# Performance work log

Measured on AMD Instinct MI355X. Metric: run time of the kernel, lower is better.

Reference implementation:

```python
import jax, jax.numpy as jnp
import numpy as np

LEVEL = 256
BLOCKS = 8
THRESH = 10.0


def setup_inputs() -> dict:
    key = jax.random.key(0)
    img = jax.random.randint(key, (16, 1024, 1024), 0, LEVEL).astype(jnp.float32)
    return {"img": img}


def _clahe(img):
    B, H, W = img.shape
    bm, bn = H // BLOCKS, W // BLOCKS
    v = img.astype(jnp.int32)  # pixel values 0..255, used as histogram bins

    # ---- per-block histograms via one flat scatter-add (segment_sum) ----
    bi = jnp.arange(H) // bm                      # block row per pixel row
    bj = jnp.arange(W) // bn                      # block col per pixel col
    blk = bi[:, None] * BLOCKS + bj[None, :]      # [H, W] block id
    seg = (jnp.arange(B)[:, None, None] * (BLOCKS * BLOCKS) + blk[None]) * LEVEL + v
    hists = jax.ops.segment_sum(
        jnp.ones((B * H * W,), jnp.float32), seg.reshape(-1),
        num_segments=B * BLOCKS * BLOCKS * LEVEL)
    hists = hists.reshape(B, BLOCKS, BLOCKS, LEVEL)

    # ---- clip histogram: redistribute excess above threshold uniformly ----
    # threshold_value = sum(hists)/LEVEL*threshold ; block sum is bm*bn exactly
    tv = (bm * bn) / LEVEL * THRESH
    total_extra = jnp.sum(jnp.maximum(hists - tv, 0.0), axis=-1, keepdims=True)
    mean_extra = total_extra / LEVEL
    # int() truncation of non-negative values == floor
    clip = jnp.floor(jnp.where(hists >= tv, tv + mean_extra, hists + mean_extra))

    # ---- CDF -> uint8 mapping table per block ----
    cdf = jnp.cumsum(clip, axis=-1) * ((LEVEL - 1) / (bm * bn))
    maps = (jnp.floor(cdf).astype(jnp.int32) % 256).astype(jnp.float32)  # [B,BLOCKS,BLOCKS,LEVEL]

    # ---- per-pixel bilinear blend of 2x2 neighboring block maps ----
    ii = jnp.arange(H, dtype=jnp.float32)
    jj = jnp.arange(W, dtype=jnp.float32)
    # Python int() truncates toward zero, so r,c are always >= 0
    r = jnp.trunc((ii - bm / 2) / bm).astype(jnp.int32)   # [H]
    c = jnp.trunc((jj - bn / 2) / bn).astype(jnp.int32)   # [W]
    x1 = (ii - (r.astype(jnp.float32) + 0.5) * bm) / bm   # [H]
    y1 = (jj - (c.astype(jnp.float32) + 0.5) * bn) / bn   # [W]
    rp = jnp.minimum(r + 1, BLOCKS - 1)
    cp = jnp.minimum(c + 1, BLOCKS - 1)
    # on last block row/col the original falls back to 1-D / nearest interp:
    x1e = jnp.where(r >= BLOCKS - 1, 0.0, x1)[:, None]    # [H,1]
    y1e = jnp.where(c >= BLOCKS - 1, 0.0, y1)[None, :]    # [1,W]

    bidx = jnp.arange(B)[:, None, None]

    def gather(rr, cc):  # maps[b, rr[i], cc[j], v[b,i,j]] -> [B,H,W]
        return maps[bidx, rr[None, :, None], cc[None, None, :], v]

    lu = gather(r, c)
    lb = gather(rp, c)
    ru = gather(r, cp)
    rb = gather(rp, cp)
    out = (1 - y1e) * ((1 - x1e) * lu + x1e * lb) + y1e * ((1 - x1e) * ru + x1e * rb)
    # final .astype('uint8') cast
    return (jnp.trunc(out).astype(jnp.int32) % 256).astype(jnp.float32)


def reference(img) -> jnp.ndarray:
    return _clahe(img)
```

## Files before the change

kernel.cpp:

```cpp
#include <hip/hip_runtime.h>
#include <hip/hip_bf16.h>

#define LEVEL 256
#define BLOCKS 8

__global__ __launch_bounds__(256) void clahe_hist_kernel(const float* __restrict__ img,
                                                         float* __restrict__ maps,
                                                         unsigned char* __restrict__ u8img) {
    __shared__ int   hist[256];
    __shared__ float red[256];
    __shared__ float scan[256];
    __shared__ float s_me;

    const int t   = threadIdx.x;
    const int bid = blockIdx.x;
    const int b   = bid >> 6;
    const int blk = bid & 63;
    const int br  = blk >> 3;
    const int bc  = blk & 7;

    hist[t] = 0;
    __syncthreads();

    const size_t base = (size_t)b * 1048576 + (size_t)(br * 128) * 1024 + (size_t)(bc * 128);
    const float* p = img + base;
    unsigned char* q8 = u8img ? (u8img + base) : nullptr;
    for (int it = 0; it < 16; ++it) {
        int idx = it * 256 + t;
        int y   = idx >> 5;
        int x   = (idx & 31) * 4;
        float4 v = *(const float4*)(p + (size_t)y * 1024 + x);
        int va = (int)v.x, vb = (int)v.y, vc = (int)v.z, vd = (int)v.w;
        atomicAdd(&hist[va], 1);
        atomicAdd(&hist[vb], 1);
        atomicAdd(&hist[vc], 1);
        atomicAdd(&hist[vd], 1);
        if (q8) {
            uchar4 pk;
            pk.x = (unsigned char)va; pk.y = (unsigned char)vb;
            pk.z = (unsigned char)vc; pk.w = (unsigned char)vd;
            *(uchar4*)(q8 + (size_t)y * 1024 + x) = pk;
        }
    }
    __syncthreads();

    const float tv = 640.0f;
    float h = (float)hist[t];
    float extra = fmaxf(h - tv, 0.0f);
    red[t] = extra;
    __syncthreads();
    for (int off = 128; off > 0; off >>= 1) {
        if (t < off) red[t] += red[t + off];
        __syncthreads();
    }
    if (t == 0) s_me = red[0] * (1.0f / 256.0f);
    __syncthreads();
    const float me = s_me;
    float clip = floorf(((h >= tv) ? tv : h) + me);

    scan[t] = clip;
    __syncthreads();
    for (int off = 1; off < 256; off <<= 1) {
        float add = (t >= off) ? scan[t - off] : 0.0f;
        __syncthreads();
        scan[t] += add;
        __syncthreads();
    }
    float cdf = scan[t] * (255.0f / 16384.0f);
    int m = ((int)floorf(cdf)) & 255;
    maps[(size_t)bid * 256 + t] = (float)m;
}

template <bool U8>
__global__ __launch_bounds__(256) void clahe_map_kernel(const float* __restrict__ imgf,
                                                        const unsigned char* __restrict__ img8,
                                                        const float* __restrict__ maps,
                                                        float* __restrict__ out) {
#pragma clang fp contract(off)
    __shared__ float4 m4[256];

    const int t  = threadIdx.x;
    const int b  = blockIdx.z;
    const int i0 = blockIdx.y * 64;
    const int j0 = blockIdx.x * 64;

    const int r  = (i0 >= 64) ? ((i0 - 64) >> 7) : 0;
    const int c  = (j0 >= 64) ? ((j0 - 64) >> 7) : 0;
    const int rp = min(r + 1, BLOCKS - 1);
    const int cp = min(c + 1, BLOCKS - 1);
    const bool rEdge = (r >= BLOCKS - 1);
    const bool cEdge = (c >= BLOCKS - 1);

    const float* mb = maps + (size_t)b * 64 * 256;
    {
        float lu = mb[(r  * 8 + c ) * 256 + t];
        float lb = mb[(rp * 8 + c ) * 256 + t];
        float ru = mb[(r  * 8 + cp) * 256 + t];
        float rb = mb[(rp * 8 + cp) * 256 + t];
        m4[t] = make_float4(lu, lb, ru, rb);
    }
    __syncthreads();

    const size_t ibase = (size_t)b * 1048576;
    const int row_in = t >> 4;
    const int col4   = (t & 15) * 4;

    for (int it = 0; it < 4; ++it) {
        const int i = i0 + it * 16 + row_in;
        const int j = j0 + col4;

        int vv[4];
        if (U8) {
            uchar4 px = *(const uchar4*)(img8 + ibase + (size_t)i * 1024 + j);
            vv[0] = px.x; vv[1] = px.y; vv[2] = px.z; vv[3] = px.w;
        } else {
            float4 px = *(const float4*)(imgf + ibase + (size_t)i * 1024 + j);
            vv[0] = (int)px.x; vv[1] = (int)px.y; vv[2] = (int)px.z; vv[3] = (int)px.w;
        }

        const float x1  = rEdge ? 0.0f : ((float)i - (float)(r * 128 + 64)) * 0.0078125f;
        const float x0  = 1.0f - x1;

        float4 o4;
        float* ov = (float*)&o4;
        for (int k = 0; k < 4; ++k) {
            const int jj = j + k;
            const float y1 = cEdge ? 0.0f : ((float)jj - (float)(c * 128 + 64)) * 0.0078125f;
            const float4 q = m4[vv[k]];
            float o = (1.0f - y1) * (x0 * q.x + x1 * q.y)
                    + y1 * (x0 * q.z + x1 * q.w);
            ov[k] = (float)(((int)o) & 255);
        }
        *(float4*)(out + ibase + (size_t)i * 1024 + j) = o4;
    }
}

extern "C" void kernel_launch(void* const* d_in, const int* in_sizes, int n_in,
                              void* d_out, int out_size, void* d_ws, size_t ws_size,
                              hipStream_t stream) {
    const float* img = (const float*)d_in[0];
    float* out = (float*)d_out;
    float* maps = (float*)d_ws;

    const size_t maps_bytes = (size_t)1024 * 256 * sizeof(float);
    const size_t u8_bytes   = (size_t)16 * 1024 * 1024;
    const bool use_u8 = ws_size >= maps_bytes + u8_bytes;
    unsigned char* u8img = use_u8 ? ((unsigned char*)d_ws + maps_bytes) : nullptr;

    clahe_hist_kernel<<<dim3(1024), dim3(256), 0, stream>>>(img, maps, u8img);
    if (use_u8) {
        clahe_map_kernel<true><<<dim3(16, 16, 16), dim3(256), 0, stream>>>(
            nullptr, u8img, maps, out);
    } else {
        clahe_map_kernel<false><<<dim3(16, 16, 16), dim3(256), 0, stream>>>(
            img, nullptr, maps, out);
    }
}
```

Before: 124.1 us.

## Pack block maps as bytes and widen map-kernel tiles to 64x128

```diff
diff --git a/kernel.cpp b/kernel.cpp
--- a/kernel.cpp
+++ b/kernel.cpp
@@ -1,11 +1,10 @@
 #include <hip/hip_runtime.h>
-#include <hip/hip_bf16.h>
 
 #define LEVEL 256
 #define BLOCKS 8
 
 __global__ __launch_bounds__(256) void clahe_hist_kernel(const float* __restrict__ img,
-                                                         float* __restrict__ maps,
+                                                         unsigned char* __restrict__ maps8,
                                                          unsigned char* __restrict__ u8img) {
     __shared__ int   hist[256];
     __shared__ float red[256];
@@ -68,70 +67,110 @@
     }
     float cdf = scan[t] * (255.0f / 16384.0f);
     int m = ((int)floorf(cdf)) & 255;
-    maps[(size_t)bid * 256 + t] = (float)m;
+    maps8[(size_t)bid * 256 + t] = (unsigned char)m;
 }
 
 template <bool U8>
 __global__ __launch_bounds__(256) void clahe_map_kernel(const float* __restrict__ imgf,
                                                         const unsigned char* __restrict__ img8,
-                                                        const float* __restrict__ maps,
+                                                        const unsigned char* __restrict__ maps8,
                                                         float* __restrict__ out) {
 #pragma clang fp contract(off)
-    __shared__ float4 m4[256];
+    __shared__ unsigned int mL[256];
+    __shared__ unsigned int mR[256];
 
     const int t  = threadIdx.x;
     const int b  = blockIdx.z;
     const int i0 = blockIdx.y * 64;
-    const int j0 = blockIdx.x * 64;
+    const int j0 = blockIdx.x * 128;
 
     const int r  = (i0 >= 64) ? ((i0 - 64) >> 7) : 0;
-    const int c  = (j0 >= 64) ? ((j0 - 64) >> 7) : 0;
     const int rp = min(r + 1, BLOCKS - 1);
-    const int cp = min(c + 1, BLOCKS - 1);
     const bool rEdge = (r >= BLOCKS - 1);
-    const bool cEdge = (c >= BLOCKS - 1);
 
-    const float* mb = maps + (size_t)b * 64 * 256;
+    const int cL  = (j0 >= 64) ? ((j0 - 64) >> 7) : 0;
+    const int cR  = j0 >> 7;
+    const int cLp = min(cL + 1, BLOCKS - 1);
+    const int cRp = min(cR + 1, BLOCKS - 1);
+    const bool cLEdge = (cL >= BLOCKS - 1);
+    const bool cREdge = (cR >= BLOCKS - 1);
+
+    const unsigned char* mb = maps8 + (size_t)b * 64 * 256;
     {
-        float lu = mb[(r  * 8 + c ) * 256 + t];
-        float lb = mb[(rp * 8 + c ) * 256 + t];
-        float ru = mb[(r  * 8 + cp) * 256 + t];
-        float rb = mb[(rp * 8 + cp) * 256 + t];
-        m4[t] = make_float4(lu, lb, ru, rb);
+        unsigned lu = mb[(r  * 8 + cL ) * 256 + t];
+        unsigned lb = mb[(rp * 8 + cL ) * 256 + t];
+        unsigned ru = mb[(r  * 8 + cLp) * 256 + t];
+        unsigned rb = mb[(rp * 8 + cLp) * 256 + t];
+        mL[t] = lu | (lb << 8) | (ru << 16) | (rb << 24);
+        unsigned lu2 = mb[(r  * 8 + cR ) * 256 + t];
+        unsigned lb2 = mb[(rp * 8 + cR ) * 256 + t];
+        unsigned ru2 = mb[(r  * 8 + cRp) * 256 + t];
+        unsigned rb2 = mb[(rp * 8 + cRp) * 256 + t];
+        mR[t] = lu2 | (lb2 << 8) | (ru2 << 16) | (rb2 << 24);
     }
     __syncthreads();
 
     const size_t ibase = (size_t)b * 1048576;
-    const int row_in = t >> 4;
-    const int col4   = (t & 15) * 4;
+    const float rbase = (float)(r * 128 + 64);
+    const float cbaseL = (float)(cL * 128 + 64);
+    const float cbaseR = (float)(cR * 128 + 64);
 
-    for (int it = 0; it < 4; ++it) {
-        const int i = i0 + it * 16 + row_in;
-        const int j = j0 + col4;
+#pragma unroll
+    for (int it = 0; it < 2; ++it) {
+        const int idx = it * 256 + t;
+        const int row = idx >> 3;
+        const int cu  = (idx & 7) * 16;
+        const int i   = i0 + row;
+        const int j   = j0 + cu;
+        const int half = cu >> 6;
+        const unsigned int* mt = half ? mR : mL;
+        const bool  cE    = half ? cREdge : cLEdge;
+        const float cbase = half ? cbaseR : cbaseL;
 
-        int vv[4];
+        unsigned int w[4];
         if (U8) {
-            uchar4 px = *(const uchar4*)(img8 + ibase + (size_t)i * 1024 + j);
-            vv[0] = px.x; vv[1] = px.y; vv[2] = px.z; vv[3] = px.w;
+            uint4 px = *(const uint4*)(img8 + ibase + (size_t)i * 1024 + j);
+            w[0] = px.x; w[1] = px.y; w[2] = px.z; w[3] = px.w;
         } else {
-            float4 px = *(const float4*)(imgf + ibase + (size_t)i * 1024 + j);
-            vv[0] = (int)px.x; vv[1] = (int)px.y; vv[2] = (int)px.z; vv[3] = (int)px.w;
+            const float* pf = imgf + ibase + (size_t)i * 1024 + j;
+#pragma unroll
+            for (int q = 0; q < 4; ++q) {
+                float4 f = *(const float4*)(pf + q * 4);
+                w[q] = (((unsigned)(int)f.x) & 255u)
+                     | ((((unsigned)(int)f.y) & 255u) << 8)
+                     | ((((unsigned)(int)f.z) & 255u) << 16)
+                     | ((((unsigned)(int)f.w) & 255u) << 24);
+            }
         }
 
-        const float x1  = rEdge ? 0.0f : ((float)i - (float)(r * 128 + 64)) * 0.0078125f;
-        const float x0  = 1.0f - x1;
+        const float x1 = rEdge ? 0.0f : ((float)i - rbase) * 0.0078125f;
+        const float x0 = 1.0f - x1;
 
-        float4 o4;
-        float* ov = (float*)&o4;
-        for (int k = 0; k < 4; ++k) {
-            const int jj = j + k;
-            const float y1 = cEdge ? 0.0f : ((float)jj - (float)(c * 128 + 64)) * 0.0078125f;
-            const float4 q = m4[vv[k]];
-            float o = (1.0f - y1) * (x0 * q.x + x1 * q.y)
-                    + y1 * (x0 * q.z + x1 * q.w);
-            ov[k] = (float)(((int)o) & 255);
+        float o16[16];
+#pragma unroll
+        for (int q = 0; q < 4; ++q) {
+            const unsigned int wq = w[q];
+#pragma unroll
+            for (int k = 0; k < 4; ++k) {
+                const int v = (wq >> (8 * k)) & 255;
+                const unsigned m = mt[v];
+                const float lu = (float)(m & 255u);
+                const float lb = (float)((m >> 8) & 255u);
+                const float ru = (float)((m >> 16) & 255u);
+                const float rb = (float)(m >> 24);
+                const float jj = (float)(j + q * 4 + k);
+                const float y1 = cE ? 0.0f : (jj - cbase) * 0.0078125f;
+                float o = (1.0f - y1) * (x0 * lu + x1 * lb)
+                        + y1 * (x0 * ru + x1 * rb);
+                o16[q * 4 + k] = (float)(((int)o) & 255);
+            }
         }
-        *(float4*)(out + ibase + (size_t)i * 1024 + j) = o4;
+
+        float* po = out + ibase + (size_t)i * 1024 + j;
+        *(float4*)(po +  0) = make_float4(o16[ 0], o16[ 1], o16[ 2], o16[ 3]);
+        *(float4*)(po +  4) = make_float4(o16[ 4], o16[ 5], o16[ 6], o16[ 7]);
+        *(float4*)(po +  8) = make_float4(o16[ 8], o16[ 9], o16[10], o16[11]);
+        *(float4*)(po + 12) = make_float4(o16[12], o16[13], o16[14], o16[15]);
     }
 }
 
@@ -140,19 +179,19 @@
                               hipStream_t stream) {
     const float* img = (const float*)d_in[0];
     float* out = (float*)d_out;
-    float* maps = (float*)d_ws;
 
-    const size_t maps_bytes = (size_t)1024 * 256 * sizeof(float);
+    unsigned char* maps8 = (unsigned char*)d_ws;
+    const size_t maps_bytes = (size_t)1024 * 256;
     const size_t u8_bytes   = (size_t)16 * 1024 * 1024;
     const bool use_u8 = ws_size >= maps_bytes + u8_bytes;
     unsigned char* u8img = use_u8 ? ((unsigned char*)d_ws + maps_bytes) : nullptr;
 
-    clahe_hist_kernel<<<dim3(1024), dim3(256), 0, stream>>>(img, maps, u8img);
+    clahe_hist_kernel<<<dim3(1024), dim3(256), 0, stream>>>(img, maps8, u8img);
     if (use_u8) {
-        clahe_map_kernel<true><<<dim3(16, 16, 16), dim3(256), 0, stream>>>(
-            nullptr, u8img, maps, out);
+        clahe_map_kernel<true><<<dim3(8, 16, 16), dim3(256), 0, stream>>>(
+            nullptr, u8img, maps8, out);
     } else {
-        clahe_map_kernel<false><<<dim3(16, 16, 16), dim3(256), 0, stream>>>(
-            img, nullptr, maps, out);
+        clahe_map_kernel<false><<<dim3(8, 16, 16), dim3(256), 0, stream>>>(
+            img, nullptr, maps8, out);
     }
 }
```

After: 130.4 us. 5.1% more time.

## Fuse histogram and mapping into one cooperative kernel with grid sync

Applied to the files above, without the earlier changes.

```diff
diff --git a/kernel.cpp b/kernel.cpp
--- a/kernel.cpp
+++ b/kernel.cpp
@@ -1,11 +1,141 @@
 #include <hip/hip_runtime.h>
-#include <hip/hip_bf16.h>
+#include <hip/hip_cooperative_groups.h>
+
+namespace cg = cooperative_groups;
 
 #define LEVEL 256
 #define BLOCKS 8
 
+__global__ __launch_bounds__(256, 4) void clahe_fused(const float* __restrict__ img,
+                                                      float* __restrict__ out,
+                                                      unsigned char* __restrict__ maps8) {
+#pragma clang fp contract(off)
+    __shared__ unsigned int pix[4096];
+    __shared__ int   hist[256];
+    __shared__ float red[256];
+    __shared__ float scan[256];
+    __shared__ unsigned int tab[1024];
+    __shared__ float s_me;
+
+    const int t   = threadIdx.x;
+    const int bid = blockIdx.x;
+    const int b   = bid >> 6;
+    const int br  = (bid >> 3) & 7;
+    const int bc  = bid & 7;
+
+    hist[t] = 0;
+    __syncthreads();
+
+    const size_t base = (size_t)b * 1048576 + (size_t)(br * 128) * 1024 + (size_t)(bc * 128);
+    const float* p = img + base;
+#pragma unroll 4
+    for (int it = 0; it < 16; ++it) {
+        int idx = it * 256 + t;
+        int y   = idx >> 5;
+        int x   = (idx & 31) * 4;
+        float4 v = *(const float4*)(p + (size_t)y * 1024 + x);
+        int va = (int)v.x, vb = (int)v.y, vc = (int)v.z, vd = (int)v.w;
+        atomicAdd(&hist[va], 1);
+        atomicAdd(&hist[vb], 1);
+        atomicAdd(&hist[vc], 1);
+        atomicAdd(&hist[vd], 1);
+        pix[idx] = (unsigned)va | ((unsigned)vb << 8) | ((unsigned)vc << 16) | ((unsigned)vd << 24);
+    }
+    __syncthreads();
+
+    const float tv = 640.0f;
+    float h = (float)hist[t];
+    red[t] = fmaxf(h - tv, 0.0f);
+    __syncthreads();
+    for (int off = 128; off > 0; off >>= 1) {
+        if (t < off) red[t] += red[t + off];
+        __syncthreads();
+    }
+    if (t == 0) s_me = red[0] * (1.0f / 256.0f);
+    __syncthreads();
+    const float me = s_me;
+    float clip = floorf(((h >= tv) ? tv : h) + me);
+
+    scan[t] = clip;
+    __syncthreads();
+    for (int off = 1; off < 256; off <<= 1) {
+        float add = (t >= off) ? scan[t - off] : 0.0f;
+        __syncthreads();
+        scan[t] += add;
+        __syncthreads();
+    }
+    float cdf = scan[t] * (255.0f / 16384.0f);
+    int m = ((int)floorf(cdf)) & 255;
+    maps8[(size_t)bid * 256 + t] = (unsigned char)m;
+
+    __threadfence();
+    cg::this_grid().sync();
+    __threadfence();
+
+    const int r0 = (br > 0) ? (br - 1) : 0;
+    const int r1 = br;
+    const int c0 = (bc > 0) ? (bc - 1) : 0;
+    const int c1 = bc;
+    const unsigned char* mb = maps8 + (size_t)b * 16384;
+#pragma unroll
+    for (int q = 0; q < 4; ++q) {
+        int rq  = (q & 2) ? r1 : r0;
+        int cq  = (q & 1) ? c1 : c0;
+        int rpq = min(rq + 1, BLOCKS - 1);
+        int cpq = min(cq + 1, BLOCKS - 1);
+        unsigned lu = mb[(rq  * 8 + cq ) * 256 + t];
+        unsigned lb = mb[(rpq * 8 + cq ) * 256 + t];
+        unsigned ru = mb[(rq  * 8 + cpq) * 256 + t];
+        unsigned rb = mb[(rpq * 8 + cpq) * 256 + t];
+        tab[q * 256 + t] = lu | (lb << 8) | (ru << 16) | (rb << 24);
+    }
+    __syncthreads();
+
+    const int colq = (t & 31) * 4;
+    const int qj   = colq >> 6;
+    const int cq   = qj ? c1 : c0;
+    const bool cEdge = (cq >= BLOCKS - 1);
+    const float cbase = (float)(cq * 128 + 64);
+    const int jg = bc * 128 + colq;
+    float y1v[4], y0v[4];
+#pragma unroll
+    for (int k = 0; k < 4; ++k) {
+        y1v[k] = cEdge ? 0.0f : ((float)(jg + k) - cbase) * 0.0078125f;
+        y0v[k] = 1.0f - y1v[k];
+    }
+
+#pragma unroll
+    for (int it = 0; it < 16; ++it) {
+        const int qi  = (it >= 8) ? 1 : 0;
+        const int rq  = qi ? r1 : r0;
+        const bool rEdge = (rq >= BLOCKS - 1);
+        const int row = it * 8 + (t >> 5);
+        const int ig  = br * 128 + row;
+        const float x1 = rEdge ? 0.0f : ((float)ig - (float)(rq * 128 + 64)) * 0.0078125f;
+        const float x0 = 1.0f - x1;
+
+        const unsigned w = pix[it * 256 + t];
+        const unsigned* tb = &tab[(qi * 2 + qj) * 256];
+
+        float4 o4;
+        float* ov = (float*)&o4;
+#pragma unroll
+        for (int k = 0; k < 4; ++k) {
+            const int v = (w >> (8 * k)) & 255;
+            const unsigned mm = tb[v];
+            const float lu = (float)(mm & 255u);
+            const float lb = (float)((mm >> 8) & 255u);
+            const float ru = (float)((mm >> 16) & 255u);
+            const float rb = (float)(mm >> 24);
+            float o = y0v[k] * (x0 * lu + x1 * lb) + y1v[k] * (x0 * ru + x1 * rb);
+            ov[k] = (float)(((int)o) & 255);
+        }
+        *(float4*)(out + base + (size_t)row * 1024 + colq) = o4;
+    }
+}
+
 __global__ __launch_bounds__(256) void clahe_hist_kernel(const float* __restrict__ img,
-                                                         float* __restrict__ maps,
+                                                         unsigned char* __restrict__ maps8,
                                                          unsigned char* __restrict__ u8img) {
     __shared__ int   hist[256];
     __shared__ float red[256];
@@ -46,8 +176,7 @@
 
     const float tv = 640.0f;
     float h = (float)hist[t];
-    float extra = fmaxf(h - tv, 0.0f);
-    red[t] = extra;
+    red[t] = fmaxf(h - tv, 0.0f);
     __syncthreads();
     for (int off = 128; off > 0; off >>= 1) {
         if (t < off) red[t] += red[t + off];
@@ -68,13 +197,13 @@
     }
     float cdf = scan[t] * (255.0f / 16384.0f);
     int m = ((int)floorf(cdf)) & 255;
-    maps[(size_t)bid * 256 + t] = (float)m;
+    maps8[(size_t)bid * 256 + t] = (unsigned char)m;
 }
 
 template <bool U8>
 __global__ __launch_bounds__(256) void clahe_map_kernel(const float* __restrict__ imgf,
                                                         const unsigned char* __restrict__ img8,
-                                                        const float* __restrict__ maps,
+                                                        const unsigned char* __restrict__ maps8,
                                                         float* __restrict__ out) {
 #pragma clang fp contract(off)
     __shared__ float4 m4[256];
@@ -91,12 +220,12 @@
     const bool rEdge = (r >= BLOCKS - 1);
     const bool cEdge = (c >= BLOCKS - 1);
 
-    const float* mb = maps + (size_t)b * 64 * 256;
+    const unsigned char* mb = maps8 + (size_t)b * 64 * 256;
     {
-        float lu = mb[(r  * 8 + c ) * 256 + t];
-        float lb = mb[(rp * 8 + c ) * 256 + t];
-        float ru = mb[(r  * 8 + cp) * 256 + t];
-        float rb = mb[(rp * 8 + cp) * 256 + t];
+        float lu = (float)mb[(r  * 8 + c ) * 256 + t];
+        float lb = (float)mb[(rp * 8 + c ) * 256 + t];
+        float ru = (float)mb[(r  * 8 + cp) * 256 + t];
+        float rb = (float)mb[(rp * 8 + cp) * 256 + t];
         m4[t] = make_float4(lu, lb, ru, rb);
     }
     __syncthreads();
@@ -140,19 +269,25 @@
                               hipStream_t stream) {
     const float* img = (const float*)d_in[0];
     float* out = (float*)d_out;
-    float* maps = (float*)d_ws;
-
-    const size_t maps_bytes = (size_t)1024 * 256 * sizeof(float);
-    const size_t u8_bytes   = (size_t)16 * 1024 * 1024;
-    const bool use_u8 = ws_size >= maps_bytes + u8_bytes;
-    unsigned char* u8img = use_u8 ? ((unsigned char*)d_ws + maps_bytes) : nullptr;
-
-    clahe_hist_kernel<<<dim3(1024), dim3(256), 0, stream>>>(img, maps, u8img);
-    if (use_u8) {
-        clahe_map_kernel<true><<<dim3(16, 16, 16), dim3(256), 0, stream>>>(
-            nullptr, u8img, maps, out);
-    } else {
-        clahe_map_kernel<false><<<dim3(16, 16, 16), dim3(256), 0, stream>>>(
-            img, nullptr, maps, out);
-    }
-}
+    unsigned char* maps8 = (unsigned char*)d_ws;
+
+    void* args[] = {(void*)&img, (void*)&out, (void*)&maps8};
+    hipError_t e = hipLaunchCooperativeKernel((const void*)clahe_fused,
+                                              dim3(1024), dim3(256),
+                                              args, 0, stream);
+    if (e != hipSuccess) {
+        const size_t maps_bytes = (size_t)1024 * 256;
+        const size_t u8_bytes   = (size_t)16 * 1024 * 1024;
+        const bool use_u8 = ws_size >= maps_bytes + u8_bytes;
+        unsigned char* u8img = use_u8 ? ((unsigned char*)d_ws + maps_bytes) : nullptr;
+
+        clahe_hist_kernel<<<dim3(1024), dim3(256), 0, stream>>>(img, maps8, u8img);
+        if (use_u8) {
+            clahe_map_kernel<true><<<dim3(16, 16, 16), dim3(256), 0, stream>>>(
+                nullptr, u8img, maps8, out);
+        } else {
+            clahe_map_kernel<false><<<dim3(16, 16, 16), dim3(256), 0, stream>>>(
+                img, nullptr, maps8, out);
+        }
+    }
+}
```

New measurement: 285.8 us. +130.3%, slower.
